# Performance work log

Hardware: AMD Instinct MI355X
Metric: run time of the kernel (lower is better)

## Reference

```python
import jax, jax.numpy as jnp
import numpy as np

B, T, D, E = 8, 4096, 128, 16
TOP_K = 2


def setup_inputs() -> dict:
    key = jax.random.key(0)
    k1, k2, k3 = jax.random.split(key, 3)
    x = jax.random.normal(k1, (B, T, D), dtype=jnp.float32)
    Wg = jax.random.normal(k2, (D, E), dtype=jnp.float32) * 0.08   # gate Dense kernel
    bg = jnp.zeros((E,), dtype=jnp.float32)                         # gate Dense bias
    Ew = jax.random.normal(k3, (E, D, D), dtype=jnp.float32) * (1.0 / np.sqrt(D))  # expert weights
    return {"x": x, "Wg": Wg, "bg": bg, "Ew": Ew}


def reference(x, Wg, bg, Ew):
    # gate: Dense(n_experts, softmax) on x (context defaults to x)
    gate_scores = jax.nn.softmax(x @ Wg + bg, axis=-1)              # (B,T,E)
    top_vals, top_idx = jax.lax.top_k(gate_scores, TOP_K)           # (B,T,2)
    top_w = top_vals / (jnp.sum(top_vals, axis=-1, keepdims=True) + 1e-6)
    # all-expert transform (faithful to original dense einsum)
    expert_outputs = jnp.einsum('btd,edo->bteo', x, Ew)             # (B,T,E,D)
    # combine top-k one-hot masks with normalized weights -> per-expert weight
    onehot = jax.nn.one_hot(top_idx, E, dtype=x.dtype)              # (B,T,2,E)
    mask = jnp.sum(onehot * top_w[..., None], axis=2)               # (B,T,E)
    m = mask[..., None]                                             # (B,T,E,1)
    weighted_avg = jnp.sum(expert_outputs * m, axis=2)              # (B,T,D)
    diff_sq = jnp.square(expert_outputs - weighted_avg[:, :, None, :])
    weighted_var = jnp.sum(diff_sq * m, axis=2)                     # (B,T,D)
    consensus = jnp.exp(-jnp.mean(weighted_var, axis=-1))           # (B,T)
    return (weighted_avg, consensus)
```

## Files before the change

kernel.cpp:

```cpp
#include <hip/hip_runtime.h>
#include <hip/hip_bf16.h>

#define NTOK 32768
#define DD 128
#define NE 16
#define CSTRIDE 32

#define OFF_COUNTS 0
#define OFF_TOKW   (4*1024)
#define OFF_LISTS  (512*1024)
#define OFF_XB     (3*1024*1024)
#define OFF_EWT    (11*1024*1024)
#define OFF_YBUF   (12*1024*1024)

typedef __attribute__((ext_vector_type(8))) short bf16x8;
typedef __attribute__((ext_vector_type(4))) float f32x4;

static __device__ inline ushort f2bf(float f) {
    uint u = __builtin_bit_cast(uint, f);
    u = u + 0x7FFFu + ((u >> 16) & 1u);
    return (ushort)(u >> 16);
}
static __device__ inline float b2f(ushort h) {
    uint u = ((uint)h) << 16;
    return __builtin_bit_cast(float, u);
}

__global__ __launch_bounds__(256) void ewt_kernel(
    const float* __restrict__ Ew, ushort* __restrict__ ewT)
{
    __shared__ float tile[32][33];
    const int b = blockIdx.x;
    const int e = b >> 4, ki = ((b >> 2) & 3) * 32, oi = (b & 3) * 32;
    const int tid = threadIdx.x;
    const int r = tid >> 3, c4 = (tid & 7) * 4;
    const float4 v = *(const float4*)(Ew + (size_t)e * DD * DD + (ki + r) * DD + oi + c4);
    tile[r][c4 + 0] = v.x; tile[r][c4 + 1] = v.y;
    tile[r][c4 + 2] = v.z; tile[r][c4 + 3] = v.w;
    __syncthreads();
    const int o = tid >> 3, k4 = (tid & 7) * 4;
    ushort4 s;
    s.x = f2bf(tile[k4 + 0][o]);
    s.y = f2bf(tile[k4 + 1][o]);
    s.z = f2bf(tile[k4 + 2][o]);
    s.w = f2bf(tile[k4 + 3][o]);
    *(ushort4*)(ewT + (size_t)e * DD * DD + (oi + o) * DD + ki + k4) = s;
}

__global__ __launch_bounds__(256) void gate_kernel(
    const float* __restrict__ x, const float* __restrict__ Wg,
    const float* __restrict__ bg,
    int* __restrict__ counts, int* __restrict__ lists, float* __restrict__ tokw,
    ushort* __restrict__ xb)
{
    __shared__ float sWgT[NE][DD];
    __shared__ float sBg[NE];
    __shared__ int   sCnt[NE];
    __shared__ int   sBase[NE];
    const int tid = threadIdx.x;
    for (int i = tid; i < DD * NE; i += 256) {
        int d = i & 127, e = i >> 7;
        sWgT[e][d] = Wg[d * NE + e];
    }
    if (tid < NE) { sBg[tid] = bg[tid]; sCnt[tid] = 0; }
    __syncthreads();

    const int t = blockIdx.x * 64 + (tid >> 2);
    const int g = tid & 3;
    const float* xt = x + (size_t)t * DD;
    ushort*      xo = xb + (size_t)t * DD;

    float logits[NE];
    #pragma unroll
    for (int e = 0; e < NE; ++e) logits[e] = 0.0f;

    #pragma unroll
    for (int i = 0; i < 8; ++i) {
        const int d0 = g * 4 + i * 16;
        float4 v = ((const float4*)xt)[g + i * 4];
        #pragma unroll
        for (int e = 0; e < NE; ++e) {
            float4 w4 = *(const float4*)&sWgT[e][d0];
            float a = logits[e];
            a = fmaf(v.x, w4.x, a);
            a = fmaf(v.y, w4.y, a);
            a = fmaf(v.z, w4.z, a);
            a = fmaf(v.w, w4.w, a);
            logits[e] = a;
        }
        ushort4 s; s.x = f2bf(v.x); s.y = f2bf(v.y); s.z = f2bf(v.z); s.w = f2bf(v.w);
        *(ushort4*)(xo + d0) = s;
    }

    #pragma unroll
    for (int e = 0; e < NE; ++e) {
        float a = logits[e];
        a += __shfl_xor(a, 1);
        a += __shfl_xor(a, 2);
        logits[e] = a + sBg[e];
    }

    float m = logits[0];
    #pragma unroll
    for (int e = 1; e < NE; ++e) m = fmaxf(m, logits[e]);
    float Z = 0.0f;
    #pragma unroll
    for (int e = 0; e < NE; ++e) Z += expf(logits[e] - m);

    int i1 = 0; float l1 = logits[0];
    #pragma unroll
    for (int e = 1; e < NE; ++e) if (logits[e] > l1) { l1 = logits[e]; i1 = e; }
    int i2 = -1; float l2 = -3.4e38f;
    #pragma unroll
    for (int e = 0; e < NE; ++e) if (e != i1 && logits[e] > l2) { l2 = logits[e]; i2 = e; }

    int s1 = 0, s2 = 0;
    if (g == 0) {
        float p1 = expf(l1 - m) / Z;
        float p2 = expf(l2 - m) / Z;
        float s  = p1 + p2 + 1e-6f;
        tokw[t * 2 + 0] = p1 / s;
        tokw[t * 2 + 1] = p2 / s;
        s1 = atomicAdd(&sCnt[i1], 1);
        s2 = atomicAdd(&sCnt[i2], 1);
    }
    __syncthreads();
    if (tid < NE) sBase[tid] = atomicAdd(&counts[tid * CSTRIDE], sCnt[tid]);
    __syncthreads();
    if (g == 0) {
        lists[i1 * NTOK + sBase[i1] + s1] = t * 2 + 0;
        lists[i2 * NTOK + sBase[i2] + s2] = t * 2 + 1;
    }
}

__global__ __launch_bounds__(256) void expert_kernel(
    const ushort* __restrict__ xb, const ushort* __restrict__ ewT,
    const int* __restrict__ counts, const int* __restrict__ lists,
    ushort* __restrict__ ybuf)
{
    const int e = blockIdx.y;
    const int count = counts[e * CSTRIDE];
    const int start = blockIdx.x * 64;
    if (start >= count) return;

    const int tid  = threadIdx.x;
    const int lane = tid & 63, wv = tid >> 6;
    const int row  = lane & 15;
    const int kg   = lane >> 4;

    const int idx = start + wv * 16 + row;
    const int en  = (idx < count) ? lists[e * NTOK + idx] : -1;
    const ushort* xrow = xb + (size_t)((en < 0 ? 0 : en) >> 1) * DD;

    bf16x8 xf[4];
    #pragma unroll
    for (int k = 0; k < 4; ++k)
        xf[k] = *(const bf16x8*)(xrow + k * 32 + kg * 8);

    const ushort* ewe = ewT + (size_t)e * DD * DD;
    f32x4 acc[8];
    #pragma unroll
    for (int n = 0; n < 8; ++n) acc[n] = (f32x4)(0.0f);

    #pragma unroll
    for (int n = 0; n < 8; ++n) {
        const ushort* er = ewe + (size_t)(n * 16 + row) * DD + kg * 8;
        #pragma unroll
        for (int k = 0; k < 4; ++k) {
            bf16x8 ef = *(const bf16x8*)(er + k * 32);
            acc[n] = __builtin_amdgcn_mfma_f32_16x16x32_bf16(ef, xf[k], acc[n], 0, 0, 0);
        }
    }

    if (en >= 0) {
        ushort* yr = ybuf + (size_t)en * DD + kg * 4;
        #pragma unroll
        for (int n = 0; n < 8; ++n) {
            ushort4 s;
            s.x = f2bf(acc[n][0]); s.y = f2bf(acc[n][1]);
            s.z = f2bf(acc[n][2]); s.w = f2bf(acc[n][3]);
            *(ushort4*)(yr + n * 16) = s;
        }
    }
}

__global__ __launch_bounds__(256) void combine_kernel(
    const ushort* __restrict__ ybuf, const float* __restrict__ tokw,
    float* __restrict__ avg_out, float* __restrict__ cons_out)
{
    const int tid = threadIdx.x;
    const int lane = tid & 63, wv = tid >> 6;
    const int half = lane >> 5, hl = lane & 31;
    const int t0 = blockIdx.x * 16 + wv * 4;

    #pragma unroll
    for (int j = 0; j < 4; ++j) {
        const int t = t0 + j;
        const float w1 = tokw[t * 2 + 0];
        const float w2 = tokw[t * 2 + 1];
        const float wo = half ? w2 : w1;
        const float wx = half ? w1 : w2;

        ushort4 raw = *(const ushort4*)(ybuf + (size_t)(t * 2 + half) * DD + hl * 4);
        float o0 = b2f(raw.x), o1 = b2f(raw.y), o2 = b2f(raw.z), o3 = b2f(raw.w);
        float x0 = __shfl_xor(o0, 32);
        float x1 = __shfl_xor(o1, 32);
        float x2 = __shfl_xor(o2, 32);
        float x3 = __shfl_xor(o3, 32);

        float a0 = wo * o0 + wx * x0;
        float a1 = wo * o1 + wx * x1;
        float a2 = wo * o2 + wx * x2;
        float a3 = wo * o3 + wx * x3;
        if (half == 0) {
            float4 av; av.x = a0; av.y = a1; av.z = a2; av.w = a3;
            ((float4*)(avg_out + (size_t)t * DD))[hl] = av;
        }
        float d0 = o0 - a0, d1 = o1 - a1, d2 = o2 - a2, d3 = o3 - a3;
        float e0 = x0 - a0, e1 = x1 - a1, e2 = x2 - a2, e3 = x3 - a3;
        float v = wo * (d0*d0 + d1*d1 + d2*d2 + d3*d3)
                + wx * (e0*e0 + e1*e1 + e2*e2 + e3*e3);
        v += __shfl_xor(v, 1);
        v += __shfl_xor(v, 2);
        v += __shfl_xor(v, 4);
        v += __shfl_xor(v, 8);
        v += __shfl_xor(v, 16);
        if (lane == 0) cons_out[t] = expf(-v * (1.0f / 128.0f));
    }
}

extern "C" void kernel_launch(void* const* d_in, const int* in_sizes, int n_in,
                              void* d_out, int out_size, void* d_ws, size_t ws_size,
                              hipStream_t stream)
{
    const float* x  = (const float*)d_in[0];
    const float* Wg = (const float*)d_in[1];
    const float* bg = (const float*)d_in[2];
    const float* Ew = (const float*)d_in[3];
    float* out = (float*)d_out;

    char* ws = (char*)d_ws;
    int*    counts = (int*)(ws + OFF_COUNTS);
    float*  tokw   = (float*)(ws + OFF_TOKW);
    int*    lists  = (int*)(ws + OFF_LISTS);
    ushort* xbuf   = (ushort*)(ws + OFF_XB);
    ushort* ewT    = (ushort*)(ws + OFF_EWT);
    ushort* ybuf   = (ushort*)(ws + OFF_YBUF);

    hipMemsetAsync(counts, 0, NE * CSTRIDE * sizeof(int), stream);

    ewt_kernel<<<256, 256, 0, stream>>>(Ew, ewT);
    gate_kernel<<<NTOK / 64, 256, 0, stream>>>(x, Wg, bg, counts, lists, tokw, xbuf);
    expert_kernel<<<dim3(NTOK / 64, NE), 256, 0, stream>>>(xbuf, ewT, counts, lists, ybuf);
    combine_kernel<<<NTOK / 16, 256, 0, stream>>>(ybuf, tokw, out, out + (size_t)NTOK * DD);
}
```

Before: 121.8 us.

## Fuse combine into expert kernel via per-token atomic completion counter

Removes the separate combine kernel. Each expert block writes its bf16 output, fences, and atomically increments a per-token done counter. The second slot to finish reads the other slot's output from ybuf, then computes the weighted average and consensus in place. This saves a kernel launch and one full read of ybuf for the second slot, at the cost of atomics, threadfences and a larger memset for the counters. The finishing slot uses fp32 accumulators for its own contribution but bf16 for the other slot, which is a slight asymmetry.

```diff
diff --git a/kernel.cpp b/kernel.cpp
--- a/kernel.cpp
+++ b/kernel.cpp
@@ -7,7 +7,8 @@
 #define CSTRIDE 32
 
 #define OFF_COUNTS 0
-#define OFF_TOKW   (4*1024)
+#define OFF_DONE   (4*1024)
+#define OFF_TOKW   (256*1024)
 #define OFF_LISTS  (512*1024)
 #define OFF_XB     (3*1024*1024)
 #define OFF_EWT    (11*1024*1024)
@@ -136,7 +137,9 @@
 __global__ __launch_bounds__(256) void expert_kernel(
     const ushort* __restrict__ xb, const ushort* __restrict__ ewT,
     const int* __restrict__ counts, const int* __restrict__ lists,
-    ushort* __restrict__ ybuf)
+    const float* __restrict__ tokw,
+    ushort* __restrict__ ybuf, int* __restrict__ done,
+    float* __restrict__ avg_out, float* __restrict__ cons_out)
 {
     const int e = blockIdx.y;
     const int count = counts[e * CSTRIDE];
@@ -182,50 +185,41 @@
             *(ushort4*)(yr + n * 16) = s;
         }
     }
-}
-
-__global__ __launch_bounds__(256) void combine_kernel(
-    const ushort* __restrict__ ybuf, const float* __restrict__ tokw,
-    float* __restrict__ avg_out, float* __restrict__ cons_out)
-{
-    const int tid = threadIdx.x;
-    const int lane = tid & 63, wv = tid >> 6;
-    const int half = lane >> 5, hl = lane & 31;
-    const int t0 = blockIdx.x * 16 + wv * 4;
-
-    #pragma unroll
-    for (int j = 0; j < 4; ++j) {
-        const int t = t0 + j;
-        const float w1 = tokw[t * 2 + 0];
-        const float w2 = tokw[t * 2 + 1];
-        const float wo = half ? w2 : w1;
-        const float wx = half ? w1 : w2;
-
-        ushort4 raw = *(const ushort4*)(ybuf + (size_t)(t * 2 + half) * DD + hl * 4);
-        float o0 = b2f(raw.x), o1 = b2f(raw.y), o2 = b2f(raw.z), o3 = b2f(raw.w);
-        float x0 = __shfl_xor(o0, 32);
-        float x1 = __shfl_xor(o1, 32);
-        float x2 = __shfl_xor(o2, 32);
-        float x3 = __shfl_xor(o3, 32);
-
-        float a0 = wo * o0 + wx * x0;
-        float a1 = wo * o1 + wx * x1;
-        float a2 = wo * o2 + wx * x2;
-        float a3 = wo * o3 + wx * x3;
-        if (half == 0) {
+
+    __threadfence();
+    int old = 0;
+    if (en >= 0 && kg == 0) old = atomicAdd(&done[en >> 1], 1);
+    old = __shfl(old, row);
+
+    if (en >= 0 && old == 1) {
+        __threadfence();
+        const int t     = en >> 1;
+        const int other = en ^ 1;
+        const int sb    = en & 1;
+        const float w_own = tokw[t * 2 + sb];
+        const float w_oth = tokw[t * 2 + (sb ^ 1)];
+        const ushort* yo = ybuf + (size_t)other * DD + kg * 4;
+
+        float v = 0.0f;
+        #pragma unroll
+        for (int n = 0; n < 8; ++n) {
+            ushort4 ro = *(const ushort4*)(yo + n * 16);
+            float o0 = b2f(ro.x), o1 = b2f(ro.y), o2 = b2f(ro.z), o3 = b2f(ro.w);
+            float a0 = w_own * acc[n][0] + w_oth * o0;
+            float a1 = w_own * acc[n][1] + w_oth * o1;
+            float a2 = w_own * acc[n][2] + w_oth * o2;
+            float a3 = w_own * acc[n][3] + w_oth * o3;
             float4 av; av.x = a0; av.y = a1; av.z = a2; av.w = a3;
-            ((float4*)(avg_out + (size_t)t * DD))[hl] = av;
-        }
-        float d0 = o0 - a0, d1 = o1 - a1, d2 = o2 - a2, d3 = o3 - a3;
-        float e0 = x0 - a0, e1 = x1 - a1, e2 = x2 - a2, e3 = x3 - a3;
-        float v = wo * (d0*d0 + d1*d1 + d2*d2 + d3*d3)
-                + wx * (e0*e0 + e1*e1 + e2*e2 + e3*e3);
-        v += __shfl_xor(v, 1);
-        v += __shfl_xor(v, 2);
-        v += __shfl_xor(v, 4);
-        v += __shfl_xor(v, 8);
+            *(float4*)(avg_out + (size_t)t * DD + n * 16 + kg * 4) = av;
+            float d0 = acc[n][0] - a0, d1 = acc[n][1] - a1;
+            float d2 = acc[n][2] - a2, d3 = acc[n][3] - a3;
+            float e0 = o0 - a0, e1 = o1 - a1, e2 = o2 - a2, e3 = o3 - a3;
+            v = fmaf(w_own, d0*d0 + d1*d1 + d2*d2 + d3*d3,
+                fmaf(w_oth, e0*e0 + e1*e1 + e2*e2 + e3*e3, v));
+        }
         v += __shfl_xor(v, 16);
-        if (lane == 0) cons_out[t] = expf(-v * (1.0f / 128.0f));
+        v += __shfl_xor(v, 32);
+        if (kg == 0) cons_out[t] = expf(-v * (1.0f / 128.0f));
     }
 }
 
@@ -241,16 +235,18 @@
 
     char* ws = (char*)d_ws;
     int*    counts = (int*)(ws + OFF_COUNTS);
+    int*    done   = (int*)(ws + OFF_DONE);
     float*  tokw   = (float*)(ws + OFF_TOKW);
     int*    lists  = (int*)(ws + OFF_LISTS);
     ushort* xbuf   = (ushort*)(ws + OFF_XB);
     ushort* ewT    = (ushort*)(ws + OFF_EWT);
     ushort* ybuf   = (ushort*)(ws + OFF_YBUF);
 
-    hipMemsetAsync(counts, 0, NE * CSTRIDE * sizeof(int), stream);
+    hipMemsetAsync(ws, 0, OFF_DONE + NTOK * sizeof(int), stream);
 
     ewt_kernel<<<256, 256, 0, stream>>>(Ew, ewT);
     gate_kernel<<<NTOK / 64, 256, 0, stream>>>(x, Wg, bg, counts, lists, tokw, xbuf);
-    expert_kernel<<<dim3(NTOK / 64, NE), 256, 0, stream>>>(xbuf, ewT, counts, lists, ybuf);
-    combine_kernel<<<NTOK / 16, 256, 0, stream>>>(ybuf, tokw, out, out + (size_t)NTOK * DD);
-}
+    expert_kernel<<<dim3(NTOK / 64, NE), 256, 0, stream>>>(
+        xbuf, ewT, counts, lists, tokw, ybuf, done,
+        out, out + (size_t)NTOK * DD);
+}
```

Result: slower. 384.0 us (+215.2%).

## Fuse transpose and gate kernels, replace global atomics with per-block count headers

Applied to the files above, without the earlier changes.

Merges the expert-weight transpose and gating kernels into one launch that dispatches on block index, and drops the memset and global atomic counters. Each gate block writes its per-expert counts to a header and its entries to fixed per-block list slots. Each expert-kernel block then compacts 16 segments into shared memory and loops over 64-token tiles. This removes two launches and the global atomic contention, but expert blocks now do a variable, serial amount of work with fewer blocks in flight.

```diff
diff --git a/kernel.cpp b/kernel.cpp
--- a/kernel.cpp
+++ b/kernel.cpp
@@ -4,10 +4,10 @@
 #define NTOK 32768
 #define DD 128
 #define NE 16
-#define CSTRIDE 32
-
-#define OFF_COUNTS 0
-#define OFF_TOKW   (4*1024)
+#define NGBLK 512
+#define NSEG 16
+#define OFF_HDR    0
+#define OFF_TOKW   (64*1024)
 #define OFF_LISTS  (512*1024)
 #define OFF_XB     (3*1024*1024)
 #define OFF_EWT    (11*1024*1024)
@@ -26,38 +26,37 @@
     return __builtin_bit_cast(float, u);
 }
 
-__global__ __launch_bounds__(256) void ewt_kernel(
-    const float* __restrict__ Ew, ushort* __restrict__ ewT)
-{
-    __shared__ float tile[32][33];
-    const int b = blockIdx.x;
-    const int e = b >> 4, ki = ((b >> 2) & 3) * 32, oi = (b & 3) * 32;
-    const int tid = threadIdx.x;
-    const int r = tid >> 3, c4 = (tid & 7) * 4;
-    const float4 v = *(const float4*)(Ew + (size_t)e * DD * DD + (ki + r) * DD + oi + c4);
-    tile[r][c4 + 0] = v.x; tile[r][c4 + 1] = v.y;
-    tile[r][c4 + 2] = v.z; tile[r][c4 + 3] = v.w;
-    __syncthreads();
-    const int o = tid >> 3, k4 = (tid & 7) * 4;
-    ushort4 s;
-    s.x = f2bf(tile[k4 + 0][o]);
-    s.y = f2bf(tile[k4 + 1][o]);
-    s.z = f2bf(tile[k4 + 2][o]);
-    s.w = f2bf(tile[k4 + 3][o]);
-    *(ushort4*)(ewT + (size_t)e * DD * DD + (oi + o) * DD + ki + k4) = s;
-}
-
-__global__ __launch_bounds__(256) void gate_kernel(
+__global__ __launch_bounds__(256) void prep_kernel(
     const float* __restrict__ x, const float* __restrict__ Wg,
-    const float* __restrict__ bg,
-    int* __restrict__ counts, int* __restrict__ lists, float* __restrict__ tokw,
-    ushort* __restrict__ xb)
-{
-    __shared__ float sWgT[NE][DD];
-    __shared__ float sBg[NE];
-    __shared__ int   sCnt[NE];
-    __shared__ int   sBase[NE];
-    const int tid = threadIdx.x;
+    const float* __restrict__ bg, const float* __restrict__ Ew,
+    ushort* __restrict__ ewT, int* __restrict__ hdr, int* __restrict__ lists,
+    float* __restrict__ tokw, ushort* __restrict__ xb)
+{
+    __shared__ __align__(16) float smem[NE * DD + NE];
+    __shared__ int sCnt[NE];
+    const int bid = blockIdx.x, tid = threadIdx.x;
+
+    if (bid < 256) {
+        float (*tile)[33] = (float(*)[33])smem;
+        const int e = bid >> 4, ki = ((bid >> 2) & 3) * 32, oi = (bid & 3) * 32;
+        const int r = tid >> 3, c4 = (tid & 7) * 4;
+        const float4 v = *(const float4*)(Ew + (size_t)e * DD * DD + (ki + r) * DD + oi + c4);
+        tile[r][c4 + 0] = v.x; tile[r][c4 + 1] = v.y;
+        tile[r][c4 + 2] = v.z; tile[r][c4 + 3] = v.w;
+        __syncthreads();
+        const int o = tid >> 3, k4 = (tid & 7) * 4;
+        ushort4 s;
+        s.x = f2bf(tile[k4 + 0][o]);
+        s.y = f2bf(tile[k4 + 1][o]);
+        s.z = f2bf(tile[k4 + 2][o]);
+        s.w = f2bf(tile[k4 + 3][o]);
+        *(ushort4*)(ewT + (size_t)e * DD * DD + (oi + o) * DD + ki + k4) = s;
+        return;
+    }
+
+    const int gbid = bid - 256;
+    float (*sWgT)[DD] = (float(*)[DD])smem;
+    float* sBg = smem + NE * DD;
     for (int i = tid; i < DD * NE; i += 256) {
         int d = i & 127, e = i >> 7;
         sWgT[e][d] = Wg[d * NE + e];
@@ -65,7 +64,7 @@
     if (tid < NE) { sBg[tid] = bg[tid]; sCnt[tid] = 0; }
     __syncthreads();
 
-    const int t = blockIdx.x * 64 + (tid >> 2);
+    const int t = gbid * 64 + (tid >> 2);
     const int g = tid & 3;
     const float* xt = x + (size_t)t * DD;
     ushort*      xo = xb + (size_t)t * DD;
@@ -114,72 +113,88 @@
     #pragma unroll
     for (int e = 0; e < NE; ++e) if (e != i1 && logits[e] > l2) { l2 = logits[e]; i2 = e; }
 
-    int s1 = 0, s2 = 0;
     if (g == 0) {
         float p1 = expf(l1 - m) / Z;
         float p2 = expf(l2 - m) / Z;
         float s  = p1 + p2 + 1e-6f;
         tokw[t * 2 + 0] = p1 / s;
         tokw[t * 2 + 1] = p2 / s;
-        s1 = atomicAdd(&sCnt[i1], 1);
-        s2 = atomicAdd(&sCnt[i2], 1);
-    }
-    __syncthreads();
-    if (tid < NE) sBase[tid] = atomicAdd(&counts[tid * CSTRIDE], sCnt[tid]);
-    __syncthreads();
-    if (g == 0) {
-        lists[i1 * NTOK + sBase[i1] + s1] = t * 2 + 0;
-        lists[i2 * NTOK + sBase[i2] + s2] = t * 2 + 1;
-    }
+        int s1 = atomicAdd(&sCnt[i1], 1);
+        int s2 = atomicAdd(&sCnt[i2], 1);
+        lists[i1 * NTOK + gbid * 64 + s1] = t * 2 + 0;
+        lists[i2 * NTOK + gbid * 64 + s2] = t * 2 + 1;
+    }
+    __syncthreads();
+    if (tid < NE) hdr[tid * NGBLK + gbid] = sCnt[tid];
 }
 
 __global__ __launch_bounds__(256) void expert_kernel(
     const ushort* __restrict__ xb, const ushort* __restrict__ ewT,
-    const int* __restrict__ counts, const int* __restrict__ lists,
+    const int* __restrict__ hdr, const int* __restrict__ lists,
     ushort* __restrict__ ybuf)
 {
     const int e = blockIdx.y;
-    const int count = counts[e * CSTRIDE];
-    const int start = blockIdx.x * 64;
-    if (start >= count) return;
-
-    const int tid  = threadIdx.x;
+    const int sg = blockIdx.x;
+    __shared__ int sCnt16[NSEG];
+    __shared__ int sEnt[NSEG * 64];
+    const int tid = threadIdx.x;
+
+    if (tid < NSEG) sCnt16[tid] = hdr[e * NGBLK + sg * NSEG + tid];
+    __syncthreads();
+
+    int off[NSEG + 1];
+    off[0] = 0;
+    #pragma unroll
+    for (int s = 0; s < NSEG; ++s) off[s + 1] = off[s] + sCnt16[s];
+    const int C = off[NSEG];
+    if (C == 0) return;
+
+    #pragma unroll
+    for (int s = 0; s < NSEG; ++s) {
+        const int c = sCnt16[s];
+        const int* src = lists + e * NTOK + (sg * NSEG + s) * 64;
+        for (int i = tid; i < c; i += 256) sEnt[off[s] + i] = src[i];
+    }
+    __syncthreads();
+
     const int lane = tid & 63, wv = tid >> 6;
     const int row  = lane & 15;
     const int kg   = lane >> 4;
-
-    const int idx = start + wv * 16 + row;
-    const int en  = (idx < count) ? lists[e * NTOK + idx] : -1;
-    const ushort* xrow = xb + (size_t)((en < 0 ? 0 : en) >> 1) * DD;
-
-    bf16x8 xf[4];
-    #pragma unroll
-    for (int k = 0; k < 4; ++k)
-        xf[k] = *(const bf16x8*)(xrow + k * 32 + kg * 8);
-
     const ushort* ewe = ewT + (size_t)e * DD * DD;
-    f32x4 acc[8];
-    #pragma unroll
-    for (int n = 0; n < 8; ++n) acc[n] = (f32x4)(0.0f);
-
-    #pragma unroll
-    for (int n = 0; n < 8; ++n) {
-        const ushort* er = ewe + (size_t)(n * 16 + row) * DD + kg * 8;
-        #pragma unroll
-        for (int k = 0; k < 4; ++k) {
-            bf16x8 ef = *(const bf16x8*)(er + k * 32);
-            acc[n] = __builtin_amdgcn_mfma_f32_16x16x32_bf16(ef, xf[k], acc[n], 0, 0, 0);
-        }
-    }
-
-    if (en >= 0) {
-        ushort* yr = ybuf + (size_t)en * DD + kg * 4;
+
+    for (int base = 0; base < C; base += 64) {
+        const int idx = base + wv * 16 + row;
+        const int en  = (idx < C) ? sEnt[idx] : -1;
+        const ushort* xrow = xb + (size_t)((en < 0 ? 0 : en) >> 1) * DD;
+
+        bf16x8 xf[4];
+        #pragma unroll
+        for (int k = 0; k < 4; ++k)
+            xf[k] = *(const bf16x8*)(xrow + k * 32 + kg * 8);
+
+        f32x4 acc[8];
+        #pragma unroll
+        for (int n = 0; n < 8; ++n) acc[n] = (f32x4)(0.0f);
+
         #pragma unroll
         for (int n = 0; n < 8; ++n) {
-            ushort4 s;
-            s.x = f2bf(acc[n][0]); s.y = f2bf(acc[n][1]);
-            s.z = f2bf(acc[n][2]); s.w = f2bf(acc[n][3]);
-            *(ushort4*)(yr + n * 16) = s;
+            const ushort* er = ewe + (size_t)(n * 16 + row) * DD + kg * 8;
+            #pragma unroll
+            for (int k = 0; k < 4; ++k) {
+                bf16x8 ef = *(const bf16x8*)(er + k * 32);
+                acc[n] = __builtin_amdgcn_mfma_f32_16x16x32_bf16(ef, xf[k], acc[n], 0, 0, 0);
+            }
+        }
+
+        if (en >= 0) {
+            ushort* yr = ybuf + (size_t)en * DD + kg * 4;
+            #pragma unroll
+            for (int n = 0; n < 8; ++n) {
+                ushort4 s;
+                s.x = f2bf(acc[n][0]); s.y = f2bf(acc[n][1]);
+                s.z = f2bf(acc[n][2]); s.w = f2bf(acc[n][3]);
+                *(ushort4*)(yr + n * 16) = s;
+            }
         }
     }
 }
@@ -240,17 +255,14 @@
     float* out = (float*)d_out;
 
     char* ws = (char*)d_ws;
-    int*    counts = (int*)(ws + OFF_COUNTS);
-    float*  tokw   = (float*)(ws + OFF_TOKW);
-    int*    lists  = (int*)(ws + OFF_LISTS);
-    ushort* xbuf   = (ushort*)(ws + OFF_XB);
-    ushort* ewT    = (ushort*)(ws + OFF_EWT);
-    ushort* ybuf   = (ushort*)(ws + OFF_YBUF);
-
-    hipMemsetAsync(counts, 0, NE * CSTRIDE * sizeof(int), stream);
-
-    ewt_kernel<<<256, 256, 0, stream>>>(Ew, ewT);
-    gate_kernel<<<NTOK / 64, 256, 0, stream>>>(x, Wg, bg, counts, lists, tokw, xbuf);
-    expert_kernel<<<dim3(NTOK / 64, NE), 256, 0, stream>>>(xbuf, ewT, counts, lists, ybuf);
+    int*    hdr   = (int*)(ws + OFF_HDR);
+    float*  tokw  = (float*)(ws + OFF_TOKW);
+    int*    lists = (int*)(ws + OFF_LISTS);
+    ushort* xbuf  = (ushort*)(ws + OFF_XB);
+    ushort* ewT   = (ushort*)(ws + OFF_EWT);
+    ushort* ybuf  = (ushort*)(ws + OFF_YBUF);
+
+    prep_kernel<<<256 + NGBLK, 256, 0, stream>>>(x, Wg, bg, Ew, ewT, hdr, lists, tokw, xbuf);
+    expert_kernel<<<dim3(NGBLK / NSEG, NE), 256, 0, stream>>>(xbuf, ewT, hdr, lists, ybuf);
     combine_kernel<<<NTOK / 16, 256, 0, stream>>>(ybuf, tokw, out, out + (size_t)NTOK * DD);
 }
```

After: 108.6 us. -10.9%, faster.
